# Kernel optimization log

Measured on AMD Instinct MI355X. Metric: run time of the kernel, lower is better.

## Reference

```python
import jax, jax.numpy as jnp
import numpy as np

HEADS = 4


def setup_inputs() -> dict:
    key = jax.random.key(0)
    kx, kqkv, kbq, ko, kbo = jax.random.split(key, 5)
    B, C, H, W = 4, 256, 64, 64
    x = jax.random.normal(kx, (B, C, H, W), dtype=jnp.float32)
    # torch nn.Linear stores weight as [out_features, in_features]
    w_qkv = jax.random.normal(kqkv, (3 * C, C), dtype=jnp.float32) * (1.0 / np.sqrt(C))
    b_qkv = jax.random.normal(kbq, (3 * C,), dtype=jnp.float32) * 0.02
    w_o = jax.random.normal(ko, (C, C), dtype=jnp.float32) * (1.0 / np.sqrt(C))
    b_o = jax.random.normal(kbo, (C,), dtype=jnp.float32) * 0.02
    return {"x": x, "w_qkv": w_qkv, "b_qkv": b_qkv, "w_o": w_o, "b_o": b_o}


def reference(x, w_qkv, b_qkv, w_o, b_o):
    B, C, H, W = x.shape
    S = H * W
    hd = C // HEADS
    # (B, C, H, W) -> (B, S, C)
    xt = x.reshape(B, C, S).transpose(0, 2, 1)
    qkv = xt @ w_qkv.T + b_qkv                      # (B, S, 3C)
    q, k, v = jnp.split(qkv, 3, axis=-1)
    def to_heads(t):
        return t.reshape(B, S, HEADS, hd).transpose(0, 2, 1, 3)  # (B, h, S, hd)
    q, k, v = to_heads(q), to_heads(k), to_heads(v)
    scores = jnp.einsum('bhqd,bhkd->bhqk', q, k) / jnp.sqrt(jnp.float32(hd))
    attn = jax.nn.softmax(scores, axis=-1)          # dropout inactive (eval)
    out = jnp.einsum('bhqk,bhkd->bhqd', attn, v)    # (B, h, S, hd)
    out = out.transpose(0, 2, 1, 3).reshape(B, S, C)
    y = out @ w_o.T + b_o                            # (B, S, C)
    y = y.reshape(B, H, W, C).transpose(0, 3, 1, 2)  # (B, C, H, W)
    return y
```

## Files before the change

### kernel.cpp

```cpp
#include <hip/hip_runtime.h>
#include <stdint.h>

#define DI __device__ __forceinline__

typedef __attribute__((ext_vector_type(8))) __bf16 bf16x8;
typedef __attribute__((ext_vector_type(8))) unsigned short u16x8;
typedef __attribute__((ext_vector_type(4))) float f32x4;
typedef __attribute__((ext_vector_type(4))) uint32_t u32x4;
typedef unsigned short u16;

constexpr int Bb = 4, Cc = 256, Ss = 4096, HD = 64;
constexpr int ELEMS = Bb * Cc * Ss;

DI u16 f2bf(float f) {
  union { float f; unsigned u; } x; x.f = f;
  return (u16)((x.u + 0x7FFFu + ((x.u >> 16) & 1u)) >> 16);
}
DI uint32_t pack2bf_trunc(float a, float b) {
  union { float f; uint32_t u; } xa, xb;
  xa.f = a; xb.f = b;
  return __builtin_amdgcn_perm(xb.u, xa.u, 0x07060302u);
}
DI bf16x8 ldfrag(const u16* p) { return __builtin_bit_cast(bf16x8, *(const u16x8*)p); }

__global__ __launch_bounds__(256) void k_convw(const float* __restrict__ w1, const float* __restrict__ w2,
                                               u16* __restrict__ d1, u16* __restrict__ d2) {
  int i = blockIdx.x * 256 + threadIdx.x;
  if (i < 196608) d1[i] = f2bf(w1[i]);
  if (i < 65536) d2[i] = f2bf(w2[i]);
}

__global__ __launch_bounds__(256) void k_transpose(const float* __restrict__ x, u16* __restrict__ xt) {
  __shared__ u16 T[64][72];
  const int st = blockIdx.x, ct = blockIdx.y, b = blockIdx.z;
  const int tid = threadIdx.x;
#pragma unroll
  for (int e = 0; e < 2; e++) {
    int ss = tid + e * 256;
    int r = ss >> 3, seg = ss & 7;
    size_t base = ((size_t)(b * Cc + ct * 64 + r) << 12) + st * 64 + seg * 8;
    u16x8 t;
#pragma unroll
    for (int j = 0; j < 8; j++) t[j] = f2bf(x[base + j]);
    *(u16x8*)&T[r][seg * 8] = t;
  }
  __syncthreads();
#pragma unroll
  for (int e = 0; e < 2; e++) {
    int ss = tid + e * 256;
    int sr = ss >> 3, cseg = ss & 7;
    u16x8 o;
#pragma unroll
    for (int j = 0; j < 8; j++) o[j] = T[cseg * 8 + j][sr];
    *(u16x8*)(xt + ((size_t)(b * Ss + st * 64 + sr) << 8) + ct * 64 + cseg * 8) = o;
  }
}

DI void stage_tile(const u16* __restrict__ src, int pitch, int r0, int k0, u16 (*dst)[40], int tid) {
#pragma unroll
  for (int e = 0; e < 2; e++) {
    int c = tid + e * 256;
    int row = c >> 2, seg = c & 3;
    u16x8 t = *(const u16x8*)(src + (size_t)(r0 + row) * pitch + k0 + seg * 8);
    *(u16x8*)&dst[row][seg * 8] = t;
  }
}

__global__ __launch_bounds__(256) void k_qkv(const u16* __restrict__ xt, const u16* __restrict__ w,
                                             const float* __restrict__ bias,
                                             u16* __restrict__ q, u16* __restrict__ kk_, u16* __restrict__ vv_) {
  __shared__ u16 As[128][40], Bs[128][40];
  const int tid = threadIdx.x;
  const int wv = tid >> 6, lane = tid & 63;
  const int wm = wv >> 1, wn = wv & 1;
  const int lr = lane & 15, quad = lane >> 4;
  const int r0 = blockIdx.x * 128;
  const int j0 = blockIdx.y * 128;
  f32x4 acc[4][4] = {};
  for (int k0 = 0; k0 < 256; k0 += 32) {
    __syncthreads();
    stage_tile(xt, 256, r0, k0, As, tid);
    stage_tile(w, 256, j0, k0, Bs, tid);
    __syncthreads();
    bf16x8 a[4], b[4];
#pragma unroll
    for (int mt = 0; mt < 4; mt++) a[mt] = ldfrag(&As[wm * 64 + mt * 16 + lr][quad * 8]);
#pragma unroll
    for (int nt = 0; nt < 4; nt++) b[nt] = ldfrag(&Bs[wn * 64 + nt * 16 + lr][quad * 8]);
#pragma unroll
    for (int mt = 0; mt < 4; mt++)
#pragma unroll
      for (int nt = 0; nt < 4; nt++)
        acc[mt][nt] = __builtin_amdgcn_mfma_f32_16x16x32_bf16(a[mt], b[nt], acc[mt][nt], 0, 0, 0);
  }
#pragma unroll
  for (int nt = 0; nt < 4; nt++) {
    int j = j0 + wn * 64 + nt * 16 + lr;
    float bj = bias[j];
    int part = j >> 8, cc = j & 255, head = cc >> 6, d = cc & 63;
    u16* outp = (part == 0) ? q : (part == 1) ? kk_ : vv_;
    float sc = (part == 0) ? 0.18033688f : 1.0f;
#pragma unroll
    for (int mt = 0; mt < 4; mt++)
#pragma unroll
      for (int rg = 0; rg < 4; rg++) {
        int row = r0 + wm * 64 + mt * 16 + quad * 4 + rg;
        int b_ = row >> 12, s = row & 4095;
        outp[((size_t)((b_ * 4 + head) * Ss + s) << 6) + d] = f2bf((acc[mt][nt][rg] + bj) * sc);
      }
  }
}

__global__ __launch_bounds__(256) void k_vt(const u16* __restrict__ v, u16* __restrict__ vt) {
  __shared__ u16 T[64][72];
  const int chunk = blockIdx.x, bh = blockIdx.y;
  const int tid = threadIdx.x;
#pragma unroll
  for (int e = 0; e < 2; e++) {
    int row = (tid >> 3) + e * 32, seg = tid & 7;
    *(u16x8*)&T[row][seg * 8] =
        *(const u16x8*)(v + ((size_t)(bh * Ss + chunk * 64 + row) << 6) + seg * 8);
  }
  __syncthreads();
#pragma unroll
  for (int e = 0; e < 2; e++) {
    int d = (tid >> 3) + e * 32, seg = tid & 7;
    u16x8 o;
#pragma unroll
    for (int j = 0; j < 8; j++) {
      int slot = seg * 8 + j;
      int t = (((slot >> 5) & 1) << 1) | ((slot >> 2) & 1);
      int w6 = t * 16 + (((slot >> 3) & 3) << 2) + (slot & 3);
      o[j] = T[w6][d];
    }
    *(u16x8*)(vt + ((size_t)(bh * 64 + d) << 12) + chunk * 64 + seg * 8) = o;
  }
}

__global__ __launch_bounds__(256, 2) void k_attn(const u16* __restrict__ Q, const u16* __restrict__ K,
                                                 const u16* __restrict__ VT, u16* __restrict__ AO,
                                                 float* __restrict__ Opart, float* __restrict__ lpart,
                                                 int nsplit) {
  __shared__ u16 Kl[2][64][72];
  __shared__ u16 Vl[2][64][72];
  const int tid = threadIdx.x;
  const int wv = tid >> 6, lane = tid & 63;
  const int lr = lane & 15, quad = lane >> 4;
  const int bh = blockIdx.y;
  const int b_ = bh >> 2, head = bh & 3;
  const int qbase = blockIdx.x * 256 + wv * 64;
  const int sp = blockIdx.z;
  const int nchunk = 64 / nsplit, kcg0 = sp * nchunk;
  const u16* Qh = Q + (size_t)bh * Ss * HD;
  const u16* Kh = K + (size_t)bh * Ss * HD;
  const u16* Vh = VT + (size_t)bh * HD * Ss;

  bf16x8 qb[4][2];
#pragma unroll
  for (int nt = 0; nt < 4; nt++)
#pragma unroll
    for (int ks = 0; ks < 2; ks++)
      qb[nt][ks] = ldfrag(Qh + (size_t)(qbase + nt * 16 + lr) * HD + ks * 32 + quad * 8);

  u16x8 ov;
#pragma unroll
  for (int j = 0; j < 8; j++) ov[j] = 0x3F80;
  const bf16x8 ones = __builtin_bit_cast(bf16x8, ov);

  f32x4 O[4][4] = {};
  f32x4 lacc[4] = {};

  u16x8 pf[4];
  const int srow = tid >> 3, sseg = tid & 7;
  auto load_chunk = [&](int kc) {
#pragma unroll
    for (int e = 0; e < 2; e++) {
      pf[e] = *(const u16x8*)(Kh + ((size_t)((kcg0 + kc) * 64 + srow + e * 32) << 6) + sseg * 8);
      pf[2 + e] = *(const u16x8*)(Vh + ((size_t)(srow + e * 32) << 12) + (kcg0 + kc) * 64 + sseg * 8);
    }
  };
  auto store_chunk = [&](int buf) {
#pragma unroll
    for (int e = 0; e < 2; e++) {
      *(u16x8*)&Kl[buf][srow + e * 32][sseg * 8] = pf[e];
      *(u16x8*)&Vl[buf][srow + e * 32][sseg * 8] = pf[2 + e];
    }
  };

  load_chunk(0);
  store_chunk(0);
  if (nchunk > 1) load_chunk(1);
  __syncthreads();

  for (int kc = 0; kc < nchunk; kc++) {
    const int cur = kc & 1;
    if (kc + 1 < nchunk) {
      store_chunk(cur ^ 1);
      if (kc + 2 < nchunk) load_chunk(kc + 2);
    }

    f32x4 St[4][4] = {};
#pragma unroll
    for (int ks = 0; ks < 2; ks++) {
      bf16x8 ka[4];
#pragma unroll
      for (int kt = 0; kt < 4; kt++) ka[kt] = ldfrag(&Kl[cur][kt * 16 + lr][ks * 32 + quad * 8]);
#pragma unroll
      for (int kt = 0; kt < 4; kt++)
#pragma unroll
        for (int nt = 0; nt < 4; nt++)
          St[kt][nt] = __builtin_amdgcn_mfma_f32_16x16x32_bf16(ka[kt], qb[nt][ks], St[kt][nt], 0, 0, 0);
    }

    uint32_t pk[4][4][2];
#pragma unroll
    for (int kt = 0; kt < 4; kt++)
#pragma unroll
      for (int nt = 0; nt < 4; nt++) {
        float p0 = __builtin_amdgcn_exp2f(St[kt][nt][0]);
        float p1 = __builtin_amdgcn_exp2f(St[kt][nt][1]);
        float p2 = __builtin_amdgcn_exp2f(St[kt][nt][2]);
        float p3 = __builtin_amdgcn_exp2f(St[kt][nt][3]);
        pk[kt][nt][0] = pack2bf_trunc(p0, p1);
        pk[kt][nt][1] = pack2bf_trunc(p2, p3);
      }

#pragma unroll
    for (int ks = 0; ks < 2; ks++) {
      bf16x8 pa[4];
#pragma unroll
      for (int mt = 0; mt < 4; mt++) {
        u32x4 t = {pk[2 * ks][mt][0], pk[2 * ks][mt][1], pk[2 * ks + 1][mt][0], pk[2 * ks + 1][mt][1]};
        pa[mt] = __builtin_bit_cast(bf16x8, t);
      }
#pragma unroll
      for (int dt = 0; dt < 4; dt++) {
        bf16x8 vb = ldfrag(&Vl[cur][dt * 16 + lr][ks * 32 + quad * 8]);
#pragma unroll
        for (int mt = 0; mt < 4; mt++)
          O[mt][dt] = __builtin_amdgcn_mfma_f32_16x16x32_bf16(pa[mt], vb, O[mt][dt], 0, 0, 0);
      }
#pragma unroll
      for (int mt = 0; mt < 4; mt++)
        lacc[mt] = __builtin_amdgcn_mfma_f32_16x16x32_bf16(pa[mt], ones, lacc[mt], 0, 0, 0);
    }

    __syncthreads();
  }

  if (nsplit == 1) {
#pragma unroll
    for (int mt = 0; mt < 4; mt++)
#pragma unroll
      for (int rg = 0; rg < 4; rg++) {
        float inv = 1.0f / lacc[mt][rg];
        int s = qbase + mt * 16 + quad * 4 + rg;
#pragma unroll
        for (int dt = 0; dt < 4; dt++)
          AO[((size_t)(b_ * Ss + s) << 8) + head * 64 + dt * 16 + lr] = f2bf(O[mt][dt][rg] * inv);
      }
  } else {
    float* Op = Opart + (size_t)sp * ELEMS;
    float* lp = lpart + (size_t)sp * (16 * Ss) + bh * Ss;
    if (lr == 0) {
#pragma unroll
      for (int mt = 0; mt < 4; mt++)
#pragma unroll
        for (int rg = 0; rg < 4; rg++) lp[qbase + mt * 16 + quad * 4 + rg] = lacc[mt][rg];
    }
#pragma unroll
    for (int mt = 0; mt < 4; mt++)
#pragma unroll
      for (int rg = 0; rg < 4; rg++) {
        int s = qbase + mt * 16 + quad * 4 + rg;
#pragma unroll
        for (int dt = 0; dt < 4; dt++)
          Op[((size_t)(b_ * Ss + s) << 8) + head * 64 + dt * 16 + lr] = O[mt][dt][rg];
      }
  }
}

__global__ __launch_bounds__(512) void k_oproj(const u16* __restrict__ wo, const u16* __restrict__ ao,
                                               const float* __restrict__ Opart, const float* __restrict__ lpart,
                                               const float* __restrict__ bo, float* __restrict__ y, int nsplit) {
  __shared__ u16 As[256][40], Bs[128][40];
  const int tid = threadIdx.x;
  const int wv = tid >> 6, lane = tid & 63;
  const int wm = wv >> 1, wn = wv & 1;
  const int lr = lane & 15, quad = lane >> 4;
  const int n0 = blockIdx.x * 128;
  f32x4 acc[4][4] = {};
  for (int k0 = 0; k0 < 256; k0 += 32) {
    __syncthreads();
#pragma unroll
    for (int e = 0; e < 2; e++) {
      int c = tid + e * 512;
      int row = c >> 2, seg = c & 3;
      *(u16x8*)&As[row][seg * 8] = *(const u16x8*)(wo + row * 256 + k0 + seg * 8);
    }
    {
      int c = tid;
      int row = c >> 2, seg = c & 3;
      int bs = n0 + row, cc = k0 + seg * 8;
      u16x8 t;
      if (nsplit == 1) {
        t = *(const u16x8*)(ao + ((size_t)bs << 8) + cc);
      } else {
        int b = bs >> 12, s = bs & 4095, head = cc >> 6;
        int li = (b * 4 + head) * Ss + s;
        f32x4 o0 = {}, o1 = {};
        float l = 0.f;
        for (int j = 0; j < nsplit; j++) {
          const float* Op = Opart + (size_t)j * ELEMS + ((size_t)bs << 8) + cc;
          f32x4 a0 = *(const f32x4*)Op, a1 = *(const f32x4*)(Op + 4);
#pragma unroll
          for (int i = 0; i < 4; i++) { o0[i] += a0[i]; o1[i] += a1[i]; }
          l += lpart[(size_t)j * 16 * Ss + li];
        }
        float inv = 1.0f / l;
#pragma unroll
        for (int i = 0; i < 4; i++) { t[i] = f2bf(o0[i] * inv); t[4 + i] = f2bf(o1[i] * inv); }
      }
      *(u16x8*)&Bs[row][seg * 8] = t;
    }
    __syncthreads();
    bf16x8 a[4], b[4];
#pragma unroll
    for (int mt = 0; mt < 4; mt++) a[mt] = ldfrag(&As[wm * 64 + mt * 16 + lr][quad * 8]);
#pragma unroll
    for (int nt = 0; nt < 4; nt++) b[nt] = ldfrag(&Bs[wn * 64 + nt * 16 + lr][quad * 8]);
#pragma unroll
    for (int mt = 0; mt < 4; mt++)
#pragma unroll
      for (int nt = 0; nt < 4; nt++)
        acc[mt][nt] = __builtin_amdgcn_mfma_f32_16x16x32_bf16(a[mt], b[nt], acc[mt][nt], 0, 0, 0);
  }
#pragma unroll
  for (int mt = 0; mt < 4; mt++)
#pragma unroll
    for (int rg = 0; rg < 4; rg++) {
      int c = wm * 64 + mt * 16 + quad * 4 + rg;
      float bc = bo[c];
#pragma unroll
      for (int nt = 0; nt < 4; nt++) {
        int col = n0 + wn * 64 + nt * 16 + lr;
        int b_ = col >> 12, s = col & 4095;
        y[((size_t)(b_ * Cc + c) << 12) + s] = acc[mt][nt][rg] + bc;
      }
    }
}

extern "C" void kernel_launch(void* const* d_in, const int* in_sizes, int n_in,
                              void* d_out, int out_size, void* d_ws, size_t ws_size,
                              hipStream_t stream) {
  const float* x = (const float*)d_in[0];
  const float* w_qkv = (const float*)d_in[1];
  const float* b_qkv = (const float*)d_in[2];
  const float* w_o = (const float*)d_in[3];
  const float* b_o = (const float*)d_in[4];
  float* y = (float*)d_out;
  u16* ws = (u16*)d_ws;
  u16* xt = ws;
  u16* q = ws + (size_t)ELEMS;
  u16* k = ws + (size_t)2 * ELEMS;
  u16* vt = ws + (size_t)3 * ELEMS;
  u16* ao = xt;
  u16* wqb = ws + (size_t)4 * ELEMS;
  u16* wob = wqb + 196608;
  const size_t Wu16 = (size_t)4 * ELEMS + 262144;
  float* Opart = (float*)(ws + Wu16);
  u16* v = (u16*)Opart;
  const size_t base = Wu16 * 2;
  auto need = [&](int n) { return base + (size_t)n * ELEMS * 4 + (size_t)n * 16 * Ss * 4; };
  const int nsplit = (ws_size >= need(2)) ? 2 : 1;
  float* lpart = Opart + (size_t)nsplit * ELEMS;

  k_convw<<<768, 256, 0, stream>>>(w_qkv, w_o, wqb, wob);
  k_transpose<<<dim3(64, 4, 4), 256, 0, stream>>>(x, xt);
  k_qkv<<<dim3(128, 6), 256, 0, stream>>>(xt, wqb, b_qkv, q, k, v);
  k_vt<<<dim3(64, 16), 256, 0, stream>>>(v, vt);
  k_attn<<<dim3(16, 16, nsplit), 256, 0, stream>>>(q, k, vt, ao, Opart, lpart, nsplit);
  k_oproj<<<128, 512, 0, stream>>>(wob, ao, Opart, lpart, b_o, y, nsplit);
}
```

Measured before the change: 184.7 us.

## Store split-attention partials as normalized bf16, fuse weight conversion, swizzle transposes

Each attention split now normalizes its partial output and stores it as bf16 instead of fp32, halving partial-output traffic. The o-proj prologue merges the two partials with weights l_j/(l0+l1). Weight conversion to bf16 is folded into the transpose kernel, which removes one launch. The LDS tiles in the transpose and V-transpose kernels get an XOR swizzle to cut bank conflicts. The cost is an extra bf16 rounding of the partials, and the merge now hardcodes two splits.

```diff
diff --git a/kernel.cpp b/kernel.cpp
--- a/kernel.cpp
+++ b/kernel.cpp
@@ -12,6 +12,7 @@
 constexpr int Bb = 4, Cc = 256, Ss = 4096, HD = 64;
 constexpr int ELEMS = Bb * Cc * Ss;
 
+DI float bf2f(u16 h) { union { unsigned u; float f; } x; x.u = ((unsigned)h) << 16; return x.f; }
 DI u16 f2bf(float f) {
   union { float f; unsigned u; } x; x.f = f;
   return (u16)((x.u + 0x7FFFu + ((x.u >> 16) & 1u)) >> 16);
@@ -23,17 +24,18 @@
 }
 DI bf16x8 ldfrag(const u16* p) { return __builtin_bit_cast(bf16x8, *(const u16x8*)p); }
 
-__global__ __launch_bounds__(256) void k_convw(const float* __restrict__ w1, const float* __restrict__ w2,
-                                               u16* __restrict__ d1, u16* __restrict__ d2) {
-  int i = blockIdx.x * 256 + threadIdx.x;
-  if (i < 196608) d1[i] = f2bf(w1[i]);
-  if (i < 65536) d2[i] = f2bf(w2[i]);
-}
-
-__global__ __launch_bounds__(256) void k_transpose(const float* __restrict__ x, u16* __restrict__ xt) {
+__global__ __launch_bounds__(256) void k_transpose(const float* __restrict__ x, u16* __restrict__ xt,
+                                                   const float* __restrict__ wq, const float* __restrict__ wo,
+                                                   u16* __restrict__ wqb, u16* __restrict__ wob) {
   __shared__ u16 T[64][72];
   const int st = blockIdx.x, ct = blockIdx.y, b = blockIdx.z;
   const int tid = threadIdx.x;
+  {
+    int flat = blockIdx.x + 64 * blockIdx.y + 256 * blockIdx.z;
+    int widx = flat * 256 + tid;
+    if (widx < 196608) wqb[widx] = f2bf(wq[widx]);
+    else wob[widx - 196608] = f2bf(wo[widx - 196608]);
+  }
 #pragma unroll
   for (int e = 0; e < 2; e++) {
     int ss = tid + e * 256;
@@ -42,7 +44,7 @@
     u16x8 t;
 #pragma unroll
     for (int j = 0; j < 8; j++) t[j] = f2bf(x[base + j]);
-    *(u16x8*)&T[r][seg * 8] = t;
+    *(u16x8*)&T[r][(seg ^ ((r >> 3) & 7)) * 8] = t;
   }
   __syncthreads();
 #pragma unroll
@@ -51,7 +53,10 @@
     int sr = ss >> 3, cseg = ss & 7;
     u16x8 o;
 #pragma unroll
-    for (int j = 0; j < 8; j++) o[j] = T[cseg * 8 + j][sr];
+    for (int j = 0; j < 8; j++) {
+      int row = cseg * 8 + j;
+      o[j] = T[row][(((sr >> 3) ^ cseg) * 8) + (sr & 7)];
+    }
     *(u16x8*)(xt + ((size_t)(b * Ss + st * 64 + sr) << 8) + ct * 64 + cseg * 8) = o;
   }
 }
@@ -118,7 +123,7 @@
 #pragma unroll
   for (int e = 0; e < 2; e++) {
     int row = (tid >> 3) + e * 32, seg = tid & 7;
-    *(u16x8*)&T[row][seg * 8] =
+    *(u16x8*)&T[row][(seg ^ ((row >> 3) & 7)) * 8] =
         *(const u16x8*)(v + ((size_t)(bh * Ss + chunk * 64 + row) << 6) + seg * 8);
   }
   __syncthreads();
@@ -131,7 +136,7 @@
       int slot = seg * 8 + j;
       int t = (((slot >> 5) & 1) << 1) | ((slot >> 2) & 1);
       int w6 = t * 16 + (((slot >> 3) & 3) << 2) + (slot & 3);
-      o[j] = T[w6][d];
+      o[j] = T[w6][(((d >> 3) ^ ((w6 >> 3) & 7)) * 8) + (d & 7)];
     }
     *(u16x8*)(vt + ((size_t)(bh * 64 + d) << 12) + chunk * 64 + seg * 8) = o;
   }
@@ -139,7 +144,7 @@
 
 __global__ __launch_bounds__(256, 2) void k_attn(const u16* __restrict__ Q, const u16* __restrict__ K,
                                                  const u16* __restrict__ VT, u16* __restrict__ AO,
-                                                 float* __restrict__ Opart, float* __restrict__ lpart,
+                                                 u16* __restrict__ AOP, float* __restrict__ lpart,
                                                  int nsplit) {
   __shared__ u16 Kl[2][64][72];
   __shared__ u16 Vl[2][64][72];
@@ -248,40 +253,28 @@
     __syncthreads();
   }
 
-  if (nsplit == 1) {
+  u16* dst = (nsplit == 1) ? AO : (AOP + (size_t)sp * ELEMS);
+  if (nsplit > 1 && lr == 0) {
+    float* lp = lpart + (size_t)sp * (16 * Ss) + bh * Ss;
 #pragma unroll
     for (int mt = 0; mt < 4; mt++)
 #pragma unroll
-      for (int rg = 0; rg < 4; rg++) {
-        float inv = 1.0f / lacc[mt][rg];
-        int s = qbase + mt * 16 + quad * 4 + rg;
-#pragma unroll
-        for (int dt = 0; dt < 4; dt++)
-          AO[((size_t)(b_ * Ss + s) << 8) + head * 64 + dt * 16 + lr] = f2bf(O[mt][dt][rg] * inv);
-      }
-  } else {
-    float* Op = Opart + (size_t)sp * ELEMS;
-    float* lp = lpart + (size_t)sp * (16 * Ss) + bh * Ss;
-    if (lr == 0) {
-#pragma unroll
-      for (int mt = 0; mt < 4; mt++)
-#pragma unroll
-        for (int rg = 0; rg < 4; rg++) lp[qbase + mt * 16 + quad * 4 + rg] = lacc[mt][rg];
-    }
-#pragma unroll
-    for (int mt = 0; mt < 4; mt++)
-#pragma unroll
-      for (int rg = 0; rg < 4; rg++) {
-        int s = qbase + mt * 16 + quad * 4 + rg;
-#pragma unroll
-        for (int dt = 0; dt < 4; dt++)
-          Op[((size_t)(b_ * Ss + s) << 8) + head * 64 + dt * 16 + lr] = O[mt][dt][rg];
-      }
-  }
+      for (int rg = 0; rg < 4; rg++) lp[qbase + mt * 16 + quad * 4 + rg] = lacc[mt][rg];
+  }
+#pragma unroll
+  for (int mt = 0; mt < 4; mt++)
+#pragma unroll
+    for (int rg = 0; rg < 4; rg++) {
+      float inv = 1.0f / lacc[mt][rg];
+      int s = qbase + mt * 16 + quad * 4 + rg;
+#pragma unroll
+      for (int dt = 0; dt < 4; dt++)
+        dst[((size_t)(b_ * Ss + s) << 8) + head * 64 + dt * 16 + lr] = f2bf(O[mt][dt][rg] * inv);
+    }
 }
 
 __global__ __launch_bounds__(512) void k_oproj(const u16* __restrict__ wo, const u16* __restrict__ ao,
-                                               const float* __restrict__ Opart, const float* __restrict__ lpart,
+                                               const u16* __restrict__ AOP, const float* __restrict__ lpart,
                                                const float* __restrict__ bo, float* __restrict__ y, int nsplit) {
   __shared__ u16 As[256][40], Bs[128][40];
   const int tid = threadIdx.x;
@@ -299,8 +292,7 @@
       *(u16x8*)&As[row][seg * 8] = *(const u16x8*)(wo + row * 256 + k0 + seg * 8);
     }
     {
-      int c = tid;
-      int row = c >> 2, seg = c & 3;
+      int row = tid >> 2, seg = tid & 3;
       int bs = n0 + row, cc = k0 + seg * 8;
       u16x8 t;
       if (nsplit == 1) {
@@ -308,18 +300,13 @@
       } else {
         int b = bs >> 12, s = bs & 4095, head = cc >> 6;
         int li = (b * 4 + head) * Ss + s;
-        f32x4 o0 = {}, o1 = {};
-        float l = 0.f;
-        for (int j = 0; j < nsplit; j++) {
-          const float* Op = Opart + (size_t)j * ELEMS + ((size_t)bs << 8) + cc;
-          f32x4 a0 = *(const f32x4*)Op, a1 = *(const f32x4*)(Op + 4);
-#pragma unroll
-          for (int i = 0; i < 4; i++) { o0[i] += a0[i]; o1[i] += a1[i]; }
-          l += lpart[(size_t)j * 16 * Ss + li];
-        }
-        float inv = 1.0f / l;
-#pragma unroll
-        for (int i = 0; i < 4; i++) { t[i] = f2bf(o0[i] * inv); t[4 + i] = f2bf(o1[i] * inv); }
+        u16x8 a0 = *(const u16x8*)(AOP + ((size_t)bs << 8) + cc);
+        u16x8 a1 = *(const u16x8*)(AOP + (size_t)ELEMS + ((size_t)bs << 8) + cc);
+        float l0 = lpart[li], l1 = lpart[16 * Ss + li];
+        float inv = 1.0f / (l0 + l1);
+        float w0 = l0 * inv, w1 = l1 * inv;
+#pragma unroll
+        for (int i = 0; i < 8; i++) t[i] = f2bf(w0 * bf2f(a0[i]) + w1 * bf2f(a1[i]));
       }
       *(u16x8*)&Bs[row][seg * 8] = t;
     }
@@ -368,17 +355,15 @@
   u16* wqb = ws + (size_t)4 * ELEMS;
   u16* wob = wqb + 196608;
   const size_t Wu16 = (size_t)4 * ELEMS + 262144;
-  float* Opart = (float*)(ws + Wu16);
-  u16* v = (u16*)Opart;
-  const size_t base = Wu16 * 2;
-  auto need = [&](int n) { return base + (size_t)n * ELEMS * 4 + (size_t)n * 16 * Ss * 4; };
-  const int nsplit = (ws_size >= need(2)) ? 2 : 1;
-  float* lpart = Opart + (size_t)nsplit * ELEMS;
-
-  k_convw<<<768, 256, 0, stream>>>(w_qkv, w_o, wqb, wob);
-  k_transpose<<<dim3(64, 4, 4), 256, 0, stream>>>(x, xt);
+  u16* aop = ws + Wu16;
+  u16* v = aop;
+  float* lpart = (float*)(aop + (size_t)2 * ELEMS);
+  const size_t need = (Wu16 + (size_t)2 * ELEMS) * 2 + (size_t)2 * 16 * Ss * 4;
+  const int nsplit = (ws_size >= need) ? 2 : 1;
+
+  k_transpose<<<dim3(64, 4, 4), 256, 0, stream>>>(x, xt, w_qkv, w_o, wqb, wob);
   k_qkv<<<dim3(128, 6), 256, 0, stream>>>(xt, wqb, b_qkv, q, k, v);
   k_vt<<<dim3(64, 16), 256, 0, stream>>>(v, vt);
-  k_attn<<<dim3(16, 16, nsplit), 256, 0, stream>>>(q, k, vt, ao, Opart, lpart, nsplit);
-  k_oproj<<<128, 512, 0, stream>>>(wob, ao, Opart, lpart, b_o, y, nsplit);
-}
+  k_attn<<<dim3(16, 16, nsplit), 256, 0, stream>>>(q, k, vt, ao, aop, lpart, nsplit);
+  k_oproj<<<128, 512, 0, stream>>>(wob, ao, aop, lpart, b_o, y, nsplit);
+}
```

Result: faster. 177.1 us (-4.1%).
